# Kernel optimization log

Measured on AMD Instinct MI355X. Metric: run time of the kernel, lower is better.

The kernel has to match this reference:

```python
import jax, jax.numpy as jnp
import numpy as np
from jax import lax

N = 10000      # nodes (also LSTM seq_len, batch=1)
E = 640000     # edges
D = 256        # num_node_features
H = 512        # hidden_size (GIN out / LSTM input)
LH = 512       # lstm_hidden_size
BN_EPS = 1e-5


def setup_inputs() -> dict:
    key = jax.random.key(0)
    ks = jax.random.split(key, 20)
    def lin(k, out_d, in_d):
        s = 1.0 / np.sqrt(in_d)
        return jax.random.uniform(k, (out_d, in_d), jnp.float32, -s, s)
    def vec(k, d, fan):
        s = 1.0 / np.sqrt(fan)
        return jax.random.uniform(k, (d,), jnp.float32, -s, s)
    inp = {
        "x": jax.random.normal(ks[0], (N, D), jnp.float32),
        "edge_index": jax.random.randint(ks[1], (2, E), 0, N, jnp.int64),
        # GIN MLP: Linear(D,H) -> ReLU -> Linear(H,H)
        "w1": lin(ks[2], H, D), "b1": vec(ks[3], H, D),
        "w2": lin(ks[4], H, H), "b2": vec(ks[5], H, H),
        # BatchNorm1d(H) affine params (training-mode batch stats)
        "gamma": jnp.ones((H,), jnp.float32), "beta": jnp.zeros((H,), jnp.float32),
        # LSTM layer 0 (input H) and layer 1 (input LH); torch gate order i,f,g,o
        "w_ih0": lin(ks[6], 4 * LH, H), "w_hh0": lin(ks[7], 4 * LH, LH),
        "b_ih0": vec(ks[8], 4 * LH, LH), "b_hh0": vec(ks[9], 4 * LH, LH),
        "w_ih1": lin(ks[10], 4 * LH, LH), "w_hh1": lin(ks[11], 4 * LH, LH),
        "b_ih1": vec(ks[12], 4 * LH, LH), "b_hh1": vec(ks[13], 4 * LH, LH),
        # fc head
        "fc_w": lin(ks[14], 1, LH), "fc_b": vec(ks[15], 1, LH),
    }
    return inp


def _lstm_layer(xs, w_ih, w_hh, b_ih, b_hh):
    # xs: [T, in]; batch=1 squeezed. Precompute input projection as one big GEMM.
    Hh = w_hh.shape[1]
    pre = xs @ w_ih.T + b_ih + b_hh  # [T, 4H]
    def step(carry, p):
        h, c = carry
        gates = p + h @ w_hh.T
        i, f, g, o = jnp.split(gates, 4)
        i = jax.nn.sigmoid(i); f = jax.nn.sigmoid(f)
        g = jnp.tanh(g); o = jax.nn.sigmoid(o)
        c = f * c + i * g
        h = o * jnp.tanh(c)
        return (h, c), h
    init = (jnp.zeros((Hh,), xs.dtype), jnp.zeros((Hh,), xs.dtype))
    (h, c), hs = lax.scan(step, init, pre)
    return hs, h, c


def reference(x, edge_index, w1, b1, w2, b2, gamma, beta,
              w_ih0, w_hh0, b_ih0, b_hh0, w_ih1, w_hh1, b_ih1, b_hh1,
              fc_w, fc_b):
    n = x.shape[0]
    src, dst = edge_index[0], edge_index[1]
    # GINConv, eps=0: h_i = MLP(x_i + sum_{j->i} x_j)
    agg = jax.ops.segment_sum(x[src], dst, num_segments=n)
    h = x + agg
    h = jax.nn.relu(h @ w1.T + b1) @ w2.T + b2  # [N, H]
    # BatchNorm1d, training mode: biased batch stats over nodes
    mean = h.mean(axis=0)
    var = h.var(axis=0)
    h = (h - mean) * lax.rsqrt(var + BN_EPS) * gamma + beta
    h = jax.nn.relu(h)
    # dropout(p=0.5) treated as identity (eval mode, deterministic reference)
    # LSTM over the node sequence (batch=1), 2 stacked layers
    hs0, h0, c0 = _lstm_layer(h, w_ih0, w_hh0, b_ih0, b_hh0)
    hs1, h1, c1 = _lstm_layer(hs0, w_ih1, w_hh1, b_ih1, b_hh1)
    out = hs1 @ fc_w.T + fc_b          # [N, 1]
    out = out[:, 0][None, :]           # [1, N] after squeeze(2)
    h_n = jnp.stack([h0, h1])[:, None, :]  # [num_layers, 1, LH]
    c_n = jnp.stack([c0, c1])[:, None, :]
    return out, h_n, c_n
```

## Files before the change

### kernel.cpp

```cpp
#include <hip/hip_runtime.h>
#include <stdint.h>

#define N_NODES 10000
#define E_EDGES 640000
#define D_IN    256
#define H_DIM   512
#define K0      64
#define K1      128
#define RING    64

typedef unsigned short ushort_t;
typedef unsigned int   uint32;
typedef unsigned long long u64;

__device__ __forceinline__ float bf2f(ushort_t u) {
  union { uint32 i; float f; } v; v.i = ((uint32)u) << 16; return v.f;
}
__device__ __forceinline__ ushort_t f2bf(float f) {
  union { float f; uint32 i; } v; v.f = f;
  uint32 x = v.i;
  uint32 r = (x + 0x7FFFu + ((x >> 16) & 1u)) >> 16;
  return (ushort_t)r;
}

__device__ __forceinline__ float sigmoid_f(float x) {
  return 1.f / (1.f + __expf(-x));
}
__device__ __forceinline__ float tanh_f(float x) {
  x = fminf(10.f, fmaxf(-10.f, x));
  float e2 = __expf(2.f * x);
  return (e2 - 1.f) / (e2 + 1.f);
}

__device__ __forceinline__ u64 ld_c8(const u64* p) {
  return __hip_atomic_load(p, __ATOMIC_RELAXED, __HIP_MEMORY_SCOPE_AGENT);
}
__device__ __forceinline__ void st_c8(u64* p, float h, int flag) {
  u64 u = ((u64)(uint32)flag << 32) | (u64)__float_as_uint(h);
  __hip_atomic_store(p, u, __ATOMIC_RELAXED, __HIP_MEMORY_SCOPE_AGENT);
}
__device__ __forceinline__ void spin_relaxed(int* p, int target) {
  int guard = 0;
  while (__hip_atomic_load(p, __ATOMIC_RELAXED, __HIP_MEMORY_SCOPE_AGENT) < target) {
    __builtin_amdgcn_s_sleep(1);
    if (++guard > 100000000) break;
  }
  __atomic_signal_fence(__ATOMIC_ACQUIRE);
}

__global__ void k_zero(int* p) {
  p[blockIdx.x * 256 + threadIdx.x] = 0;
}

__global__ void k_detect(const int* eb, int* ctrl) {
  int v = eb[2 * (int)threadIdx.x + 1];
  if (v != 0) atomicOr(ctrl, 1);
}

__device__ __forceinline__ int edge_src(const int* eb, int flag, int e) {
  return flag ? eb[e] : eb[2 * e];
}
__device__ __forceinline__ int edge_dst(const int* eb, int flag, int e) {
  return flag ? eb[E_EDGES + e] : eb[2 * (E_EDGES + e)];
}

__global__ __launch_bounds__(256) void k_count(const int* eb, const int* ctrl, int* deg) {
  int e = blockIdx.x * 256 + threadIdx.x;
  if (e >= E_EDGES) return;
  int flag = ctrl[0];
  atomicAdd(&deg[edge_dst(eb, flag, e)], 1);
}

__global__ __launch_bounds__(1024) void k_prefix(const int* deg, int* off, int* cursor) {
  __shared__ int sums[1024];
  int tid = threadIdx.x;
  const int PER = 10;
  int base = tid * PER;
  int loc[PER];
  int s = 0;
  for (int i = 0; i < PER; i++) {
    int idx = base + i;
    int v = (idx < N_NODES) ? deg[idx] : 0;
    loc[i] = s; s += v;
  }
  sums[tid] = s;
  __syncthreads();
  for (int d = 1; d < 1024; d <<= 1) {
    int v = (tid >= d) ? sums[tid - d] : 0;
    __syncthreads();
    sums[tid] += v;
    __syncthreads();
  }
  int excl = (tid == 0) ? 0 : sums[tid - 1];
  for (int i = 0; i < PER; i++) {
    int idx = base + i;
    if (idx < N_NODES) { int o = excl + loc[i]; off[idx] = o; cursor[idx] = o; }
  }
  if (tid == 1023) off[N_NODES] = sums[1023];
}

// ... 59 lines not shown
    }
    __syncthreads();
  }
  float* Cf = (float*)Cout;
  ushort_t* Cb = (ushort_t*)Cout;
  #pragma unroll
  for (int i = 0; i < 4; i++) {
    int row = by * 64 + 16 * i + ty;
    if (row >= M) continue;
    #pragma unroll
    for (int j = 0; j < 4; j++) {
      int col = bn * 64 + 16 * j + tx;
      float b = bias1[col];
      if (TWOBIAS) b += bias2[col];
      float v = acc[i][j] + b;
      if (RELU) v = fmaxf(v, 0.f);
      if (OUTBF16) Cb[(size_t)row * Ncols + col] = f2bf(v);
      else         Cf[(size_t)row * Ncols + col] = v;
    }
  }
}

__global__ __launch_bounds__(256) void k_bnstats(const float* y2, float* colsum, float* colsumsq) {
  int b = blockIdx.x, tid = threadIdx.x;
  int r0 = b * 64, r1 = min(r0 + 64, N_NODES);
  float s0 = 0, q0 = 0, s1 = 0, q1 = 0;
  for (int r = r0; r < r1; r++) {
    float v0 = y2[(size_t)r * H_DIM + tid];
    float v1 = y2[(size_t)r * H_DIM + tid + 256];
    s0 += v0; q0 += v0 * v0; s1 += v1; q1 += v1 * v1;
  }
  atomicAdd(&colsum[tid], s0);        atomicAdd(&colsumsq[tid], q0);
  atomicAdd(&colsum[tid + 256], s1);  atomicAdd(&colsumsq[tid + 256], q1);
}

__global__ __launch_bounds__(256) void k_bnfin(float* colsum, float* colsumsq,
                                               const float* gamma, const float* beta) {
  int c = blockIdx.x * 256 + threadIdx.x;
  if (c >= H_DIM) return;
  float mean = colsum[c] * (1.f / N_NODES);
  float var  = colsumsq[c] * (1.f / N_NODES) - mean * mean;
  float sc = gamma[c] * rsqrtf(var + 1e-5f);
  float sh = beta[c] - mean * sc;
  colsum[c] = sc; colsumsq[c] = sh;
}

__global__ __launch_bounds__(256) void k_bnapply(float* y2, const float* sc, const float* sh) {
  size_t i = (size_t)blockIdx.x * 256 + threadIdx.x;
  int c = (int)(i & (H_DIM - 1));
  float v = y2[i] * sc[c] + sh[c];
  y2[i] = v > 0.f ? v : 0.f;
}

__global__ __launch_bounds__(256, 1) void k_lstm(const ushort_t* pre0, const float* w_hh0,
                                              const float* w_ih1, const float* w_hh1,
                                              const float* b_ih1, const float* b_hh1,
                                              u64* hs0c, u64* hs1c, float* hs1p,
                                              int* flags1, float* dout) {
  __shared__ float lds_in[2][512];
  __shared__ float lds_dots[32];
  __shared__ float lds_pre[2][32];
  int tid = threadIdx.x;
  int wave = tid >> 6, lane = tid & 63;
  int kp = lane & 7;
  int r = wave * 8 + (lane >> 3);
  int wg = blockIdx.x;

  float w_reg[64];
  float c_reg = 0.f;

  if (wg < K0) {
    int u0 = wg * 8;
    {
      int grow = (r >> 3) * H_DIM + u0 + (r & 7);
      const float* src = w_hh0 + (size_t)grow * H_DIM + kp * 64;
      #pragma unroll
      for (int i = 0; i < 16; i++) {
        int j0 = ((i + 2 * kp) & 15) * 4;
        float4 v = *(const float4*)(src + j0);
        w_reg[4 * i + 0] = v.x; w_reg[4 * i + 1] = v.y;
        w_reg[4 * i + 2] = v.z; w_reg[4 * i + 3] = v.w;
      }
    }
    float pf = 0.f;
    if (tid < 32)
      pf = bf2f(pre0[(tid >> 3) * H_DIM + u0 + (tid & 7)]);

    for (int t = 0; t < N_NODES; t++) {
      int phase = t & 1;
      if (t > 0) {
        const u64* pa = hs0c + ((t - 1) & (RING - 1)) * 512 + tid;
        const u64* pb = pa + 256;
        u64 ua, ub; int guard = 0;
        for (;;) {
          ua = ld_c8(pa); ub = ld_c8(pb);
          if (((int)(ua >> 32) == t && (int)(ub >> 32) == t) || ++guard > 100000000) break;
        }
        lds_in[0][tid]       = __uint_as_float((uint32)ua);
        lds_in[0][tid + 256] = __uint_as_float((uint32)ub);
      }
      if (tid < 32) lds_pre[phase][tid] = pf;
      __syncthreads();
      if (tid < 32 && t + 1 < N_NODES)
        pf = bf2f(pre0[(size_t)(t + 1) * 2048 + (tid >> 3) * H_DIM + u0 + (tid & 7)]);
      if ((t & 31) == 0 && t >= RING && tid < K1)
        spin_relaxed(&flags1[tid * 16], t - 32);
      if (t > 0) {
        const float* hrow = &lds_in[0][kp * 64];
        float dot = 0.f;
        #pragma unroll
        for (int i = 0; i < 16; i++) {
          int j0 = ((i + 2 * kp) & 15) * 4;
          float4 h4 = *(const float4*)(hrow + j0);
          dot += w_reg[4 * i] * h4.x + w_reg[4 * i + 1] * h4.y
               + w_reg[4 * i + 2] * h4.z + w_reg[4 * i + 3] * h4.w;
        }
        dot += __shfl_xor(dot, 1, 64);
        dot += __shfl_xor(dot, 2, 64);
        dot += __shfl_xor(dot, 4, 64);
        if (kp == 0) lds_dots[r] = dot;
      } else if (tid < 32) {
        lds_dots[tid] = 0.f;
      }
      __syncthreads();
      if (wave == 0) {
        float val = 0.f;
        if (lane < 32) {
          float pre = lds_dots[lane] + lds_pre[phase][lane];
          val = ((lane >> 3) == 2) ? tanh_f(pre) : sigmoid_f(pre);
        }
        int j = lane & 7;
        float ii = __shfl(val, j, 64);
        float ff = __shfl(val, 8 + j, 64);
        float gg = __shfl(val, 16 + j, 64);
        float oo = __shfl(val, 24 + j, 64);
        if (lane < 8) {
          c_reg = ff * c_reg + ii * gg;
          float hv = oo * tanh_f(c_reg);
          st_c8(hs0c + (t & (RING - 1)) * 512 + u0 + lane, hv, t + 1);
          if (t == N_NODES - 1) {
            dout[10000 + u0 + lane] = hv;
            dout[11024 + u0 + lane] = c_reg;
          }
        }
      }
    }
  } else {
    int wg1 = wg - K0;
    int u0 = wg1 * 4;
    int m = r >> 4;
    {
      int gj = r & 15;
      int grow = (gj >> 2) * H_DIM + u0 + (gj & 3);
      const float* src = (m ? w_hh1 : w_ih1) + (size_t)grow * H_DIM + kp * 64;
      #pragma unroll
      for (int i = 0; i < 16; i++) {
        int j0 = ((i + 2 * kp) & 15) * 4;
        float4 v = *(const float4*)(src + j0);
        w_reg[4 * i + 0] = v.x; w_reg[4 * i + 1] = v.y;
        w_reg[4 * i + 2] = v.z; w_reg[4 * i + 3] = v.w;
      }
    }
    if (tid < 16) {
      int g = tid >> 2, j = tid & 3;
      int grow = g * H_DIM + u0 + j;
      lds_pre[0][tid] = b_ih1[grow] + b_hh1[grow];
    }
    __syncthreads();

    for (int s = 0; s < N_NODES; s++) {
      {
        bool need1 = (s > 0);
        const u64* p0a = hs0c + (s & (RING - 1)) * 512 + tid;
        const u64* p0b = p0a + 256;
        const u64* p1a = hs1c + ((s - 1) & (RING - 1)) * 512 + tid;
        const u64* p1b = p1a + 256;
        u64 u0a, u0b, u1a, u1b; int guard = 0;
        for (;;) {
          u0a = ld_c8(p0a); u0b = ld_c8(p0b);
          u1a = ld_c8(p1a); u1b = ld_c8(p1b);
          bool ok0 = ((int)(u0a >> 32) == s + 1) && ((int)(u0b >> 32) == s + 1);
          bool ok1 = !need1 || (((int)(u1a >> 32) == s) && ((int)(u1b >> 32) == s));
          if ((ok0 && ok1) || ++guard > 100000000) break;
        }
        if (!need1) { u1a = 0; u1b = 0; }
        lds_in[0][tid]       = __uint_as_float((uint32)u0a);
        lds_in[0][tid + 256] = __uint_as_float((uint32)u0b);
        lds_in[1][tid]       = __uint_as_float((uint32)u1a);
        lds_in[1][tid + 256] = __uint_as_float((uint32)u1b);
      }
      __syncthreads();
      if (tid == 0)
        __hip_atomic_store(&flags1[wg1 * 16], s + 1, __ATOMIC_RELAXED, __HIP_MEMORY_SCOPE_AGENT);
      {
        const float* hrow = &lds_in[m][kp * 64];
        float dot = 0.f;
        #pragma unroll
        for (int i = 0; i < 16; i++) {
          int j0 = ((i + 2 * kp) & 15) * 4;
          float4 h4 = *(const float4*)(hrow + j0);
          dot += w_reg[4 * i] * h4.x + w_reg[4 * i + 1] * h4.y
               + w_reg[4 * i + 2] * h4.z + w_reg[4 * i + 3] * h4.w;
        }
        dot += __shfl_xor(dot, 1, 64);
        dot += __shfl_xor(dot, 2, 64);
        dot += __shfl_xor(dot, 4, 64);
        if (kp == 0) lds_dots[r] = dot;
      }
      __syncthreads();
      if (wave == 0) {
        float val = 0.f;
        if (lane < 16) {
          float pre = lds_dots[lane] + lds_dots[16 + lane] + lds_pre[0][lane];
          val = ((lane >> 2) == 2) ? tanh_f(pre) : sigmoid_f(pre);
        }
        int j = lane & 3;
        float ii = __shfl(val, j, 64);
        float ff = __shfl(val, 4 + j, 64);
        float gg = __shfl(val, 8 + j, 64);
        float oo = __shfl(val, 12 + j, 64);
        if (lane < 4) {
          c_reg = ff * c_reg + ii * gg;
          float hv = oo * tanh_f(c_reg);
          st_c8(hs1c + (s & (RING - 1)) * 512 + u0 + lane, hv, s + 1);
          hs1p[(size_t)s * H_DIM + u0 + lane] = hv;
          if (s == N_NODES - 1) {
            dout[10512 + u0 + lane] = hv;
            dout[11536 + u0 + lane] = c_reg;
          }
        }
      }
    }
  }
}

__global__ __launch_bounds__(256) void k_fc(const float* hs1, const float* fc_w,
                                            const float* fc_b, float* dout) {
  int row = blockIdx.x * 4 + (threadIdx.x >> 6);
  int lane = threadIdx.x & 63;
  float acc = 0.f;
  #pragma unroll
  for (int j = 0; j < 8; j++) {
    int c = lane + 64 * j;
    acc += hs1[(size_t)row * H_DIM + c] * fc_w[c];
  }
  for (int d = 32; d; d >>= 1) acc += __shfl_xor(acc, d, 64);
  if (lane == 0) dout[row] = acc + fc_b[0];
}

extern "C" void kernel_launch(void* const* d_in, const int* in_sizes, int n_in,
                              void* d_out, int out_size, void* d_ws, size_t ws_size,
                              hipStream_t stream) {
  const float* x     = (const float*)d_in[0];
  const int*   eb    = (const int*)d_in[1];
  const float* w1    = (const float*)d_in[2];
  const float* b1    = (const float*)d_in[3];
  const float* w2    = (const float*)d_in[4];
  const float* b2    = (const float*)d_in[5];
  const float* gamma = (const float*)d_in[6];
  const float* beta  = (const float*)d_in[7];
  const float* w_ih0 = (const float*)d_in[8];
  const float* w_hh0 = (const float*)d_in[9];
  const float* b_ih0 = (const float*)d_in[10];
  const float* b_hh0 = (const float*)d_in[11];
  const float* w_ih1 = (const float*)d_in[12];
  const float* w_hh1 = (const float*)d_in[13];
  const float* b_ih1 = (const float*)d_in[14];
  const float* b_hh1 = (const float*)d_in[15];
  const float* fc_w  = (const float*)d_in[16];
  const float* fc_b  = (const float*)d_in[17];
  float* dout = (float*)d_out;
  char* ws = (char*)d_ws;

  int*    ctrl     = (int*)(ws + 0);
  int*    flags1   = (int*)(ws + 256);
  float*  colsum   = (float*)(ws + 8448);
  float*  colsumsq = (float*)(ws + 10496);
  int*    deg      = (int*)(ws + 12544);
  u64*    hs0c     = (u64*)(ws + 57344);
  u64*    hs1c     = (u64*)(ws + 319488);
  float*  y1       = (float*)(ws + 581632);
  float*  y2       = (float*)(ws + 21061632);
  float*  h0       = y2;
  ushort_t* pre0   = (ushort_t*)(ws + 41541632);
  int*    off      = (int*)(ws + 41541632);
  int*    cursor   = (int*)(ws + 41582080);
  int*    csr      = (int*)(ws + 41622528);
  float*  hs1p     = y1;

  k_zero<<<56, 256, 0, stream>>>((int*)ws);
  k_detect<<<1, 64, 0, stream>>>(eb, ctrl);
  k_count<<<2500, 256, 0, stream>>>(eb, ctrl, deg);
  k_prefix<<<1, 1024, 0, stream>>>(deg, off, cursor);
  k_fill<<<2500, 256, 0, stream>>>(eb, ctrl, cursor, csr);
  k_agg<<<10000, 256, 0, stream>>>(x, off, csr, h0);

  dim3 g1(157, 8);
  k_gemm<256, true,  false, false><<<g1, 256, 0, stream>>>(h0, w1, b1, nullptr, y1, N_NODES, 512);
  dim3 g2(157, 8);
  k_gemm<512, false, false, false><<<g2, 256, 0, stream>>>(y1, w2, b2, nullptr, y2, N_NODES, 512);

  k_bnstats<<<157, 256, 0, stream>>>(y2, colsum, colsumsq);
  k_bnfin<<<2, 256, 0, stream>>>(colsum, colsumsq, gamma, beta);
  k_bnapply<<<20000, 256, 0, stream>>>(y2, colsum, colsumsq);

  dim3 g3(157, 32);
  k_gemm<512, false, true, true><<<g3, 256, 0, stream>>>(y2, w_ih0, b_ih0, b_hh0, pre0, N_NODES, 2048);

  k_lstm<<<192, 256, 0, stream>>>(pre0, w_hh0, w_ih1, w_hh1, b_ih1, b_hh1,
                                  hs0c, hs1c, hs1p, flags1, dout);
  k_fc<<<2500, 256, 0, stream>>>(hs1p, fc_w, fc_b, dout);
}
```

Baseline: 26.20 ms.

## Restructure persistent LSTM into single-wave workgroups with no LDS or barriers

Splits the persistent two-layer LSTM into 512 single-wavefront workgroups: 256 for layer 0 and 256 for layer 1, each owning 2 hidden units. Each lane holds an 8-wide slice of the weight rows in registers and reads its h slice straight from the flagged global ring, so the LDS staging and both __syncthreads per step go away. Dot products are reduced with full-wave shuffles, and the layer-0 throttle on layer-1 progress now uses a wave-wide vote every 16 steps. In exchange every wave polls the ring separately, which adds polling traffic, and the butterfly reductions cost more shuffles per step. The workspace offsets are also reshuffled.

Result: slower. 38.68 ms (+47.6%).

```diff
diff --git a/kernel.cpp b/kernel.cpp
--- a/kernel.cpp
+++ b/kernel.cpp
@@ -5,8 +5,6 @@
 #define E_EDGES 640000
 #define D_IN    256
 #define H_DIM   512
-#define K0      64
-#define K1      128
 #define RING    64
 
 typedef unsigned short ushort_t;
@@ -38,14 +36,6 @@
 __device__ __forceinline__ void st_c8(u64* p, float h, int flag) {
   u64 u = ((u64)(uint32)flag << 32) | (u64)__float_as_uint(h);
   __hip_atomic_store(p, u, __ATOMIC_RELAXED, __HIP_MEMORY_SCOPE_AGENT);
-}
-__device__ __forceinline__ void spin_relaxed(int* p, int target) {
-  int guard = 0;
-  while (__hip_atomic_load(p, __ATOMIC_RELAXED, __HIP_MEMORY_SCOPE_AGENT) < target) {
-    __builtin_amdgcn_s_sleep(1);
-    if (++guard > 100000000) break;
-  }
-  __atomic_signal_fence(__ATOMIC_ACQUIRE);
 }
 
 __global__ void k_zero(int* p) {
@@ -211,184 +201,220 @@
   y2[i] = v > 0.f ? v : 0.f;
 }
 
-__global__ __launch_bounds__(256, 1) void k_lstm(const ushort_t* pre0, const float* w_hh0,
+__global__ __launch_bounds__(64, 1) void k_lstm(const ushort_t* pre0, const float* w_hh0,
                                               const float* w_ih1, const float* w_hh1,
                                               const float* b_ih1, const float* b_hh1,
                                               u64* hs0c, u64* hs1c, float* hs1p,
                                               int* flags1, float* dout) {
-  __shared__ float lds_in[2][512];
-  __shared__ float lds_dots[32];
-  __shared__ float lds_pre[2][32];
-  int tid = threadIdx.x;
-  int wave = tid >> 6, lane = tid & 63;
-  int kp = lane & 7;
-  int r = wave * 8 + (lane >> 3);
+  int lane = threadIdx.x;
   int wg = blockIdx.x;
 
-  float w_reg[64];
-  float c_reg = 0.f;
-
-  if (wg < K0) {
-    int u0 = wg * 8;
-    {
-      int grow = (r >> 3) * H_DIM + u0 + (r & 7);
-      const float* src = w_hh0 + (size_t)grow * H_DIM + kp * 64;
+  if (wg < 256) {
+    int ubase = wg * 2;
+    float wr[8][8];
+    #pragma unroll
+    for (int rr = 0; rr < 8; rr++) {
+      int g = rr >> 1, u = rr & 1;
+      const float* src = w_hh0 + (size_t)(g * H_DIM + ubase + u) * H_DIM + lane * 8;
+      float4 a = *(const float4*)(src);
+      float4 b = *(const float4*)(src + 4);
+      wr[rr][0] = a.x; wr[rr][1] = a.y; wr[rr][2] = a.z; wr[rr][3] = a.w;
+      wr[rr][4] = b.x; wr[rr][5] = b.y; wr[rr][6] = b.z; wr[rr][7] = b.w;
+    }
+    uint32 ppk[4];
+    #pragma unroll
+    for (int g = 0; g < 4; g++)
+      ppk[g] = *(const uint32*)(pre0 + (size_t)0 * 2048 + g * H_DIM + ubase);
+    float c0 = 0.f, c1 = 0.f;
+
+    for (int t = 0; t < N_NODES; t++) {
+      float h[8];
+      if (t > 0) {
+        const u64* base = hs0c + (size_t)((t - 1) & (RING - 1)) * 512 + lane * 8;
+        u64 cc[8]; int guard = 0;
+        for (;;) {
+          #pragma unroll
+          for (int j = 0; j < 8; j++) cc[j] = ld_c8(base + j);
+          bool ok = true;
+          #pragma unroll
+          for (int j = 0; j < 8; j++) ok = ok && ((int)(cc[j] >> 32) == t);
+          if (ok || ++guard > 50000000) break;
+        }
+        #pragma unroll
+        for (int j = 0; j < 8; j++) h[j] = __uint_as_float((uint32)cc[j]);
+      } else {
+        #pragma unroll
+        for (int j = 0; j < 8; j++) h[j] = 0.f;
+      }
+      uint32 ppn[4];
+      if (t + 1 < N_NODES) {
+        #pragma unroll
+        for (int g = 0; g < 4; g++)
+          ppn[g] = *(const uint32*)(pre0 + (size_t)(t + 1) * 2048 + g * H_DIM + ubase);
+      } else {
+        #pragma unroll
+        for (int g = 0; g < 4; g++) ppn[g] = 0;
+      }
+      float d[8];
+      if (t > 0) {
+        #pragma unroll
+        for (int rr = 0; rr < 8; rr++) {
+          float s = 0.f;
+          #pragma unroll
+          for (int j = 0; j < 8; j++) s += wr[rr][j] * h[j];
+          d[rr] = s;
+        }
+        #pragma unroll
+        for (int rr = 0; rr < 8; rr++) {
+          #pragma unroll
+          for (int off = 1; off < 64; off <<= 1) d[rr] += __shfl_xor(d[rr], off, 64);
+        }
+      } else {
+        #pragma unroll
+        for (int rr = 0; rr < 8; rr++) d[rr] = 0.f;
+      }
+      float h0v, h1v;
+      {
+        float gi = d[0] + bf2f((ushort_t)(ppk[0] & 0xFFFF));
+        float gf = d[2] + bf2f((ushort_t)(ppk[1] & 0xFFFF));
+        float gg = d[4] + bf2f((ushort_t)(ppk[2] & 0xFFFF));
+        float go = d[6] + bf2f((ushort_t)(ppk[3] & 0xFFFF));
+        float ii = sigmoid_f(gi), ff = sigmoid_f(gf), g2 = tanh_f(gg), oo = sigmoid_f(go);
+        c0 = ff * c0 + ii * g2;
+        h0v = oo * tanh_f(c0);
+      }
+      {
+        float gi = d[1] + bf2f((ushort_t)(ppk[0] >> 16));
+        float gf = d[3] + bf2f((ushort_t)(ppk[1] >> 16));
+        float gg = d[5] + bf2f((ushort_t)(ppk[2] >> 16));
+        float go = d[7] + bf2f((ushort_t)(ppk[3] >> 16));
+        float ii = sigmoid_f(gi), ff = sigmoid_f(gf), g2 = tanh_f(gg), oo = sigmoid_f(go);
+        c1 = ff * c1 + ii * g2;
+        h1v = oo * tanh_f(c1);
+      }
+      if (lane < 2) {
+        float hv = lane ? h1v : h0v;
+        st_c8(hs0c + (size_t)(t & (RING - 1)) * 512 + ubase + lane, hv, t + 1);
+        if (t == N_NODES - 1) {
+          dout[10000 + ubase + lane] = hv;
+          dout[11024 + ubase + lane] = lane ? c1 : c0;
+        }
+      }
+      if ((t & 15) == 0 && t >= 48) {
+        int tgt = t - 32;
+        int g2_ = 0;
+        for (;;) {
+          int m0 = __hip_atomic_load(&flags1[lane * 4 + 0], __ATOMIC_RELAXED, __HIP_MEMORY_SCOPE_AGENT);
+          int m1 = __hip_atomic_load(&flags1[lane * 4 + 1], __ATOMIC_RELAXED, __HIP_MEMORY_SCOPE_AGENT);
+          int m2 = __hip_atomic_load(&flags1[lane * 4 + 2], __ATOMIC_RELAXED, __HIP_MEMORY_SCOPE_AGENT);
+          int m3 = __hip_atomic_load(&flags1[lane * 4 + 3], __ATOMIC_RELAXED, __HIP_MEMORY_SCOPE_AGENT);
+          bool myok = (m0 >= tgt) && (m1 >= tgt) && (m2 >= tgt) && (m3 >= tgt);
+          if (__all(myok) || ++g2_ > 5000000) break;
+          __builtin_amdgcn_s_sleep(1);
+        }
+      }
       #pragma unroll
-      for (int i = 0; i < 16; i++) {
-        int j0 = ((i + 2 * kp) & 15) * 4;
-        float4 v = *(const float4*)(src + j0);
-        w_reg[4 * i + 0] = v.x; w_reg[4 * i + 1] = v.y;
-        w_reg[4 * i + 2] = v.z; w_reg[4 * i + 3] = v.w;
-      }
-    }
-    float pf = 0.f;
-    if (tid < 32)
-      pf = bf2f(pre0[(tid >> 3) * H_DIM + u0 + (tid & 7)]);
-
-    for (int t = 0; t < N_NODES; t++) {
-      int phase = t & 1;
-      if (t > 0) {
-        const u64* pa = hs0c + ((t - 1) & (RING - 1)) * 512 + tid;
-        const u64* pb = pa + 256;
-        u64 ua, ub; int guard = 0;
-        for (;;) {
-          ua = ld_c8(pa); ub = ld_c8(pb);
-          if (((int)(ua >> 32) == t && (int)(ub >> 32) == t) || ++guard > 100000000) break;
-        }
-        lds_in[0][tid]       = __uint_as_float((uint32)ua);
-        lds_in[0][tid + 256] = __uint_as_float((uint32)ub);
-      }
-      if (tid < 32) lds_pre[phase][tid] = pf;
-      __syncthreads();
-      if (tid < 32 && t + 1 < N_NODES)
-        pf = bf2f(pre0[(size_t)(t + 1) * 2048 + (tid >> 3) * H_DIM + u0 + (tid & 7)]);
-      if ((t & 31) == 0 && t >= RING && tid < K1)
-        spin_relaxed(&flags1[tid * 16], t - 32);
-      if (t > 0) {
-        const float* hrow = &lds_in[0][kp * 64];
-        float dot = 0.f;
-        #pragma unroll
-        for (int i = 0; i < 16; i++) {
-          int j0 = ((i + 2 * kp) & 15) * 4;
-          float4 h4 = *(const float4*)(hrow + j0);
-          dot += w_reg[4 * i] * h4.x + w_reg[4 * i + 1] * h4.y
-               + w_reg[4 * i + 2] * h4.z + w_reg[4 * i + 3] * h4.w;
-        }
-        dot += __shfl_xor(dot, 1, 64);
-        dot += __shfl_xor(dot, 2, 64);
-        dot += __shfl_xor(dot, 4, 64);
-        if (kp == 0) lds_dots[r] = dot;
-      } else if (tid < 32) {
-        lds_dots[tid] = 0.f;
-      }
-      __syncthreads();
-      if (wave == 0) {
-        float val = 0.f;
-        if (lane < 32) {
-          float pre = lds_dots[lane] + lds_pre[phase][lane];
-          val = ((lane >> 3) == 2) ? tanh_f(pre) : sigmoid_f(pre);
-        }
-        int j = lane & 7;
-        float ii = __shfl(val, j, 64);
-        float ff = __shfl(val, 8 + j, 64);
-        float gg = __shfl(val, 16 + j, 64);
-        float oo = __shfl(val, 24 + j, 64);
-        if (lane < 8) {
-          c_reg = ff * c_reg + ii * gg;
-          float hv = oo * tanh_f(c_reg);
-          st_c8(hs0c + (t & (RING - 1)) * 512 + u0 + lane, hv, t + 1);
-          if (t == N_NODES - 1) {
-            dout[10000 + u0 + lane] = hv;
-            dout[11024 + u0 + lane] = c_reg;
+      for (int g = 0; g < 4; g++) ppk[g] = ppn[g];
+    }
+  } else {
+    int wg1 = wg - 256;
+    int ubase = wg1 * 2;
+    float wi[8][8], wh[8][8], bb[8];
+    #pragma unroll
+    for (int rr = 0; rr < 8; rr++) {
+      int g = rr >> 1, u = rr & 1;
+      size_t grow = (size_t)(g * H_DIM + ubase + u);
+      const float* si = w_ih1 + grow * H_DIM + lane * 8;
+      const float* sh = w_hh1 + grow * H_DIM + lane * 8;
+      float4 a = *(const float4*)(si);
+      float4 b = *(const float4*)(si + 4);
+      wi[rr][0] = a.x; wi[rr][1] = a.y; wi[rr][2] = a.z; wi[rr][3] = a.w;
+      wi[rr][4] = b.x; wi[rr][5] = b.y; wi[rr][6] = b.z; wi[rr][7] = b.w;
+      float4 c = *(const float4*)(sh);
+      float4 e = *(const float4*)(sh + 4);
+      wh[rr][0] = c.x; wh[rr][1] = c.y; wh[rr][2] = c.z; wh[rr][3] = c.w;
+      wh[rr][4] = e.x; wh[rr][5] = e.y; wh[rr][6] = e.z; wh[rr][7] = e.w;
+      bb[rr] = b_ih1[grow] + b_hh1[grow];
+    }
+    float c0 = 0.f, c1 = 0.f;
+
+    for (int s = 0; s < N_NODES; s++) {
+      float h0[8], h1[8];
+      {
+        const u64* b0 = hs0c + (size_t)(s & (RING - 1)) * 512 + lane * 8;
+        const u64* b1 = hs1c + (size_t)((s - 1) & (RING - 1)) * 512 + lane * 8;
+        u64 a0[8], a1[8]; int guard = 0;
+        if (s > 0) {
+          for (;;) {
+            #pragma unroll
+            for (int j = 0; j < 8; j++) a0[j] = ld_c8(b0 + j);
+            #pragma unroll
+            for (int j = 0; j < 8; j++) a1[j] = ld_c8(b1 + j);
+            bool ok = true;
+            #pragma unroll
+            for (int j = 0; j < 8; j++) ok = ok && ((int)(a0[j] >> 32) == s + 1);
+            #pragma unroll
+            for (int j = 0; j < 8; j++) ok = ok && ((int)(a1[j] >> 32) == s);
+            if (ok || ++guard > 50000000) break;
           }
-        }
-      }
-    }
-  } else {
-    int wg1 = wg - K0;
-    int u0 = wg1 * 4;
-    int m = r >> 4;
-    {
-      int gj = r & 15;
-      int grow = (gj >> 2) * H_DIM + u0 + (gj & 3);
-      const float* src = (m ? w_hh1 : w_ih1) + (size_t)grow * H_DIM + kp * 64;
+          #pragma unroll
+          for (int j = 0; j < 8; j++) { h0[j] = __uint_as_float((uint32)a0[j]); h1[j] = __uint_as_float((uint32)a1[j]); }
+        } else {
+          for (;;) {
+            #pragma unroll
+            for (int j = 0; j < 8; j++) a0[j] = ld_c8(b0 + j);
+            bool ok = true;
+            #pragma unroll
+            for (int j = 0; j < 8; j++) ok = ok && ((int)(a0[j] >> 32) == 1);
+            if (ok || ++guard > 50000000) break;
+          }
+          #pragma unroll
+          for (int j = 0; j < 8; j++) { h0[j] = __uint_as_float((uint32)a0[j]); h1[j] = 0.f; }
+        }
+      }
+      float d[8];
       #pragma unroll
-      for (int i = 0; i < 16; i++) {
-        int j0 = ((i + 2 * kp) & 15) * 4;
-        float4 v = *(const float4*)(src + j0);
-        w_reg[4 * i + 0] = v.x; w_reg[4 * i + 1] = v.y;
-        w_reg[4 * i + 2] = v.z; w_reg[4 * i + 3] = v.w;
-      }
-    }
-    if (tid < 16) {
-      int g = tid >> 2, j = tid & 3;
-      int grow = g * H_DIM + u0 + j;
-      lds_pre[0][tid] = b_ih1[grow] + b_hh1[grow];
-    }
-    __syncthreads();
-
-    for (int s = 0; s < N_NODES; s++) {
+      for (int rr = 0; rr < 8; rr++) {
+        float acc = 0.f;
+        #pragma unroll
+        for (int j = 0; j < 8; j++) acc += wi[rr][j] * h0[j];
+        #pragma unroll
+        for (int j = 0; j < 8; j++) acc += wh[rr][j] * h1[j];
+        d[rr] = acc;
+      }
+      #pragma unroll
+      for (int rr = 0; rr < 8; rr++) {
+        #pragma unroll
+        for (int off = 1; off < 64; off <<= 1) d[rr] += __shfl_xor(d[rr], off, 64);
+      }
+      float h0v, h1v;
       {
-        bool need1 = (s > 0);
-        const u64* p0a = hs0c + (s & (RING - 1)) * 512 + tid;
-        const u64* p0b = p0a + 256;
-        const u64* p1a = hs1c + ((s - 1) & (RING - 1)) * 512 + tid;
-        const u64* p1b = p1a + 256;
-        u64 u0a, u0b, u1a, u1b; int guard = 0;
-        for (;;) {
-          u0a = ld_c8(p0a); u0b = ld_c8(p0b);
-          u1a = ld_c8(p1a); u1b = ld_c8(p1b);
-          bool ok0 = ((int)(u0a >> 32) == s + 1) && ((int)(u0b >> 32) == s + 1);
-          bool ok1 = !need1 || (((int)(u1a >> 32) == s) && ((int)(u1b >> 32) == s));
-          if ((ok0 && ok1) || ++guard > 100000000) break;
-        }
-        if (!need1) { u1a = 0; u1b = 0; }
-        lds_in[0][tid]       = __uint_as_float((uint32)u0a);
-        lds_in[0][tid + 256] = __uint_as_float((uint32)u0b);
-        lds_in[1][tid]       = __uint_as_float((uint32)u1a);
-        lds_in[1][tid + 256] = __uint_as_float((uint32)u1b);
-      }
-      __syncthreads();
-      if (tid == 0)
-        __hip_atomic_store(&flags1[wg1 * 16], s + 1, __ATOMIC_RELAXED, __HIP_MEMORY_SCOPE_AGENT);
+        float ii = sigmoid_f(d[0] + bb[0]);
+        float ff = sigmoid_f(d[2] + bb[2]);
+        float g2 = tanh_f(d[4] + bb[4]);
+        float oo = sigmoid_f(d[6] + bb[6]);
+        c0 = ff * c0 + ii * g2;
+        h0v = oo * tanh_f(c0);
+      }
       {
-        const float* hrow = &lds_in[m][kp * 64];
-        float dot = 0.f;
-        #pragma unroll
-        for (int i = 0; i < 16; i++) {
-          int j0 = ((i + 2 * kp) & 15) * 4;
-          float4 h4 = *(const float4*)(hrow + j0);
-          dot += w_reg[4 * i] * h4.x + w_reg[4 * i + 1] * h4.y
-               + w_reg[4 * i + 2] * h4.z + w_reg[4 * i + 3] * h4.w;
-        }
-        dot += __shfl_xor(dot, 1, 64);
-        dot += __shfl_xor(dot, 2, 64);
-        dot += __shfl_xor(dot, 4, 64);
-        if (kp == 0) lds_dots[r] = dot;
-      }
-      __syncthreads();
-      if (wave == 0) {
-        float val = 0.f;
-        if (lane < 16) {
-          float pre = lds_dots[lane] + lds_dots[16 + lane] + lds_pre[0][lane];
-          val = ((lane >> 2) == 2) ? tanh_f(pre) : sigmoid_f(pre);
-        }
-        int j = lane & 3;
-        float ii = __shfl(val, j, 64);
-        float ff = __shfl(val, 4 + j, 64);
-        float gg = __shfl(val, 8 + j, 64);
-        float oo = __shfl(val, 12 + j, 64);
-        if (lane < 4) {
-          c_reg = ff * c_reg + ii * gg;
-          float hv = oo * tanh_f(c_reg);
-          st_c8(hs1c + (s & (RING - 1)) * 512 + u0 + lane, hv, s + 1);
-          hs1p[(size_t)s * H_DIM + u0 + lane] = hv;
-          if (s == N_NODES - 1) {
-            dout[10512 + u0 + lane] = hv;
-            dout[11536 + u0 + lane] = c_reg;
-          }
-        }
-      }
+        float ii = sigmoid_f(d[1] + bb[1]);
+        float ff = sigmoid_f(d[3] + bb[3]);
+        float g2 = tanh_f(d[5] + bb[5]);
+        float oo = sigmoid_f(d[7] + bb[7]);
+        c1 = ff * c1 + ii * g2;
+        h1v = oo * tanh_f(c1);
+      }
+      if (lane < 2) {
+        float hv = lane ? h1v : h0v;
+        st_c8(hs1c + (size_t)(s & (RING - 1)) * 512 + ubase + lane, hv, s + 1);
+        hs1p[(size_t)s * H_DIM + ubase + lane] = hv;
+        if (s == N_NODES - 1) {
+          dout[10512 + ubase + lane] = hv;
+          dout[11536 + ubase + lane] = lane ? c1 : c0;
+        }
+      }
+      if (lane == 0)
+        __hip_atomic_store(&flags1[wg1], s + 1, __ATOMIC_RELAXED, __HIP_MEMORY_SCOPE_AGENT);
     }
   }
 }
@@ -432,19 +458,19 @@
   char* ws = (char*)d_ws;
 
   int*    ctrl     = (int*)(ws + 0);
-  int*    flags1   = (int*)(ws + 256);
-  float*  colsum   = (float*)(ws + 8448);
-  float*  colsumsq = (float*)(ws + 10496);
-  int*    deg      = (int*)(ws + 12544);
-  u64*    hs0c     = (u64*)(ws + 57344);
-  u64*    hs1c     = (u64*)(ws + 319488);
-  float*  y1       = (float*)(ws + 581632);
-  float*  y2       = (float*)(ws + 21061632);
+  int*    flags1   = (int*)(ws + 1024);
+  float*  colsum   = (float*)(ws + 4096);
+  float*  colsumsq = (float*)(ws + 6144);
+  int*    deg      = (int*)(ws + 8192);
+  u64*    hs0c     = (u64*)(ws + 65536);
+  u64*    hs1c     = (u64*)(ws + 327680);
+  float*  y1       = (float*)(ws + 589824);
+  float*  y2       = (float*)(ws + 21069824);
   float*  h0       = y2;
-  ushort_t* pre0   = (ushort_t*)(ws + 41541632);
-  int*    off      = (int*)(ws + 41541632);
-  int*    cursor   = (int*)(ws + 41582080);
-  int*    csr      = (int*)(ws + 41622528);
+  ushort_t* pre0   = (ushort_t*)(ws + 41549824);
+  int*    off      = (int*)(ws + 41549824);
+  int*    cursor   = (int*)(ws + 41589828);
+  int*    csr      = (int*)(ws + 41629828);
   float*  hs1p     = y1;
 
   k_zero<<<56, 256, 0, stream>>>((int*)ws);
@@ -466,7 +492,7 @@
   dim3 g3(157, 32);
   k_gemm<512, false, true, true><<<g3, 256, 0, stream>>>(y2, w_ih0, b_ih0, b_hh0, pre0, N_NODES, 2048);
 
-  k_lstm<<<192, 256, 0, stream>>>(pre0, w_hh0, w_ih1, w_hh1, b_ih1, b_hh1,
-                                  hs0c, hs1c, hs1p, flags1, dout);
+  k_lstm<<<512, 64, 0, stream>>>(pre0, w_hh0, w_ih1, w_hh1, b_ih1, b_hh1,
+                                 hs0c, hs1c, hs1p, flags1, dout);
   k_fc<<<2500, 256, 0, stream>>>(hs1p, fc_w, fc_b, dout);
 }
```

## Remove second block barrier per LSTM step by computing gates inside each wave

Applied to the files above, without the earlier changes.

Reworks the persistent LSTM kernel so each wave owns whole hidden units (two units per wave in layer 0, one in layer 1). All four gate dot products for a unit are reduced inside the wave with shuffles, and the cell update runs there too. This removes the per-step LDS gate exchange and the second __syncthreads, and the h buffer is double-buffered in LDS. Layer-1 flags are packed densely instead of padded to 16 ints, and the layer-0 backpressure check changes to poll them with a different target and sleep. The gate activations are now computed redundantly on many lanes, and the denser flag layout may cause more contention on the polled lines.

After: 33.58 ms. 1.28x slower.

```diff
diff --git a/kernel.cpp b/kernel.cpp
--- a/kernel.cpp
+++ b/kernel.cpp
@@ -38,14 +38,6 @@
 __device__ __forceinline__ void st_c8(u64* p, float h, int flag) {
   u64 u = ((u64)(uint32)flag << 32) | (u64)__float_as_uint(h);
   __hip_atomic_store(p, u, __ATOMIC_RELAXED, __HIP_MEMORY_SCOPE_AGENT);
-}
-__device__ __forceinline__ void spin_relaxed(int* p, int target) {
-  int guard = 0;
-  while (__hip_atomic_load(p, __ATOMIC_RELAXED, __HIP_MEMORY_SCOPE_AGENT) < target) {
-    __builtin_amdgcn_s_sleep(1);
-    if (++guard > 100000000) break;
-  }
-  __atomic_signal_fence(__ATOMIC_ACQUIRE);
 }
 
 __global__ void k_zero(int* p) {
@@ -216,177 +208,168 @@
                                               const float* b_ih1, const float* b_hh1,
                                               u64* hs0c, u64* hs1c, float* hs1p,
                                               int* flags1, float* dout) {
-  __shared__ float lds_in[2][512];
-  __shared__ float lds_dots[32];
-  __shared__ float lds_pre[2][32];
+  __shared__ float lds_h[2][1024];
   int tid = threadIdx.x;
   int wave = tid >> 6, lane = tid & 63;
-  int kp = lane & 7;
-  int r = wave * 8 + (lane >> 3);
   int wg = blockIdx.x;
 
-  float w_reg[64];
-  float c_reg = 0.f;
-
   if (wg < K0) {
-    int u0 = wg * 8;
+    int u_w = wg * 8 + wave * 2;
+    int rr = lane >> 3, kp = lane & 7;
+    int g_r = rr >> 1, u_r = rr & 1;
+    float w_reg[64];
     {
-      int grow = (r >> 3) * H_DIM + u0 + (r & 7);
-      const float* src = w_hh0 + (size_t)grow * H_DIM + kp * 64;
+      const float* src = w_hh0 + (size_t)(g_r * H_DIM + u_w + u_r) * H_DIM + kp * 64;
       #pragma unroll
       for (int i = 0; i < 16; i++) {
         int j0 = ((i + 2 * kp) & 15) * 4;
         float4 v = *(const float4*)(src + j0);
-        w_reg[4 * i + 0] = v.x; w_reg[4 * i + 1] = v.y;
-        w_reg[4 * i + 2] = v.z; w_reg[4 * i + 3] = v.w;
-      }
-    }
-    float pf = 0.f;
-    if (tid < 32)
-      pf = bf2f(pre0[(tid >> 3) * H_DIM + u0 + (tid & 7)]);
+        w_reg[4*i+0]=v.x; w_reg[4*i+1]=v.y; w_reg[4*i+2]=v.z; w_reg[4*i+3]=v.w;
+      }
+    }
+    int myu = u_w + (lane & 1);
+    float ppk[4];
+    #pragma unroll
+    for (int g = 0; g < 4; g++)
+      ppk[g] = bf2f(pre0[(size_t)0 * 2048 + g * H_DIM + myu]);
+    float c_reg = 0.f;
 
     for (int t = 0; t < N_NODES; t++) {
-      int phase = t & 1;
+      float* Lh = lds_h[t & 1];
       if (t > 0) {
-        const u64* pa = hs0c + ((t - 1) & (RING - 1)) * 512 + tid;
+        const u64* pa = hs0c + (size_t)((t-1) & (RING-1)) * 512 + tid;
         const u64* pb = pa + 256;
         u64 ua, ub; int guard = 0;
         for (;;) {
           ua = ld_c8(pa); ub = ld_c8(pb);
-          if (((int)(ua >> 32) == t && (int)(ub >> 32) == t) || ++guard > 100000000) break;
-        }
-        lds_in[0][tid]       = __uint_as_float((uint32)ua);
-        lds_in[0][tid + 256] = __uint_as_float((uint32)ub);
-      }
-      if (tid < 32) lds_pre[phase][tid] = pf;
+          if (((int)(ua>>32) == t && (int)(ub>>32) == t) || ++guard > 100000000) break;
+        }
+        Lh[tid]       = __uint_as_float((uint32)ua);
+        Lh[tid + 256] = __uint_as_float((uint32)ub);
+      }
       __syncthreads();
-      if (tid < 32 && t + 1 < N_NODES)
-        pf = bf2f(pre0[(size_t)(t + 1) * 2048 + (tid >> 3) * H_DIM + u0 + (tid & 7)]);
-      if ((t & 31) == 0 && t >= RING && tid < K1)
-        spin_relaxed(&flags1[tid * 16], t - 32);
+      float ppn[4];
+      if (t + 1 < N_NODES) {
+        #pragma unroll
+        for (int g = 0; g < 4; g++)
+          ppn[g] = bf2f(pre0[(size_t)(t+1) * 2048 + g * H_DIM + myu]);
+      } else { ppn[0]=ppn[1]=ppn[2]=ppn[3]=0.f; }
+      if ((t & 31) == 0 && t >= 32 && tid < K1) {
+        int tgt = t - 31, guard = 0;
+        while (__hip_atomic_load(&flags1[tid], __ATOMIC_RELAXED, __HIP_MEMORY_SCOPE_AGENT) < tgt) {
+          __builtin_amdgcn_s_sleep(2);
+          if (++guard > 50000000) break;
+        }
+      }
+      float d = 0.f;
       if (t > 0) {
-        const float* hrow = &lds_in[0][kp * 64];
-        float dot = 0.f;
+        const float* hrow = Lh + kp * 64;
         #pragma unroll
         for (int i = 0; i < 16; i++) {
           int j0 = ((i + 2 * kp) & 15) * 4;
           float4 h4 = *(const float4*)(hrow + j0);
-          dot += w_reg[4 * i] * h4.x + w_reg[4 * i + 1] * h4.y
-               + w_reg[4 * i + 2] * h4.z + w_reg[4 * i + 3] * h4.w;
-        }
-        dot += __shfl_xor(dot, 1, 64);
-        dot += __shfl_xor(dot, 2, 64);
-        dot += __shfl_xor(dot, 4, 64);
-        if (kp == 0) lds_dots[r] = dot;
-      } else if (tid < 32) {
-        lds_dots[tid] = 0.f;
-      }
-      __syncthreads();
-      if (wave == 0) {
-        float val = 0.f;
-        if (lane < 32) {
-          float pre = lds_dots[lane] + lds_pre[phase][lane];
-          val = ((lane >> 3) == 2) ? tanh_f(pre) : sigmoid_f(pre);
-        }
-        int j = lane & 7;
-        float ii = __shfl(val, j, 64);
-        float ff = __shfl(val, 8 + j, 64);
-        float gg = __shfl(val, 16 + j, 64);
-        float oo = __shfl(val, 24 + j, 64);
-        if (lane < 8) {
-          c_reg = ff * c_reg + ii * gg;
-          float hv = oo * tanh_f(c_reg);
-          st_c8(hs0c + (t & (RING - 1)) * 512 + u0 + lane, hv, t + 1);
-          if (t == N_NODES - 1) {
-            dout[10000 + u0 + lane] = hv;
-            dout[11024 + u0 + lane] = c_reg;
-          }
-        }
-      }
+          d += w_reg[4*i]*h4.x + w_reg[4*i+1]*h4.y + w_reg[4*i+2]*h4.z + w_reg[4*i+3]*h4.w;
+        }
+        d += __shfl_xor(d, 1, 64);
+        d += __shfl_xor(d, 2, 64);
+        d += __shfl_xor(d, 4, 64);
+      }
+      int u = lane & 1;
+      float gi = __shfl(d, 8 * u, 64)      + ppk[0];
+      float gf = __shfl(d, 16 + 8 * u, 64) + ppk[1];
+      float gg = __shfl(d, 32 + 8 * u, 64) + ppk[2];
+      float go = __shfl(d, 48 + 8 * u, 64) + ppk[3];
+      float ii = sigmoid_f(gi), ff = sigmoid_f(gf), gz = tanh_f(gg), oo = sigmoid_f(go);
+      c_reg = ff * c_reg + ii * gz;
+      float hv = oo * tanh_f(c_reg);
+      if (lane < 2) {
+        st_c8(hs0c + (size_t)(t & (RING-1)) * 512 + myu, hv, t + 1);
+        if (t == N_NODES - 1) {
+          dout[10000 + myu] = hv;
+          dout[11024 + myu] = c_reg;
+        }
+      }
+      ppk[0]=ppn[0]; ppk[1]=ppn[1]; ppk[2]=ppn[2]; ppk[3]=ppn[3];
     }
   } else {
     int wg1 = wg - K0;
-    int u0 = wg1 * 4;
-    int m = r >> 4;
+    int unit = wg1 * 4 + wave;
+    int g_r = lane >> 4, seg = lane & 15;
+    float w_reg[64];
     {
-      int gj = r & 15;
-      int grow = (gj >> 2) * H_DIM + u0 + (gj & 3);
-      const float* src = (m ? w_hh1 : w_ih1) + (size_t)grow * H_DIM + kp * 64;
+      size_t grow = (size_t)(g_r * H_DIM + unit);
+      const float* base = (seg < 8) ? (w_ih1 + grow * H_DIM) : (w_hh1 + grow * H_DIM - 512);
       #pragma unroll
       for (int i = 0; i < 16; i++) {
-        int j0 = ((i + 2 * kp) & 15) * 4;
-        float4 v = *(const float4*)(src + j0);
-        w_reg[4 * i + 0] = v.x; w_reg[4 * i + 1] = v.y;
-        w_reg[4 * i + 2] = v.z; w_reg[4 * i + 3] = v.w;
-      }
-    }
-    if (tid < 16) {
-      int g = tid >> 2, j = tid & 3;
-      int grow = g * H_DIM + u0 + j;
-      lds_pre[0][tid] = b_ih1[grow] + b_hh1[grow];
-    }
-    __syncthreads();
+        int j0 = ((i + seg) & 15) * 4;
+        float4 v = *(const float4*)(base + seg * 64 + j0);
+        w_reg[4*i+0]=v.x; w_reg[4*i+1]=v.y; w_reg[4*i+2]=v.z; w_reg[4*i+3]=v.w;
+      }
+    }
+    float bb[4];
+    #pragma unroll
+    for (int g = 0; g < 4; g++) bb[g] = b_ih1[g * H_DIM + unit] + b_hh1[g * H_DIM + unit];
+    float c_reg = 0.f;
 
     for (int s = 0; s < N_NODES; s++) {
+      float* Lh = lds_h[s & 1];
       {
-        bool need1 = (s > 0);
-        const u64* p0a = hs0c + (s & (RING - 1)) * 512 + tid;
+        const u64* p0a = hs0c + (size_t)(s & (RING-1)) * 512 + tid;
         const u64* p0b = p0a + 256;
-        const u64* p1a = hs1c + ((s - 1) & (RING - 1)) * 512 + tid;
-        const u64* p1b = p1a + 256;
-        u64 u0a, u0b, u1a, u1b; int guard = 0;
-        for (;;) {
-          u0a = ld_c8(p0a); u0b = ld_c8(p0b);
-          u1a = ld_c8(p1a); u1b = ld_c8(p1b);
-          bool ok0 = ((int)(u0a >> 32) == s + 1) && ((int)(u0b >> 32) == s + 1);
-          bool ok1 = !need1 || (((int)(u1a >> 32) == s) && ((int)(u1b >> 32) == s));
-          if ((ok0 && ok1) || ++guard > 100000000) break;
-        }
-        if (!need1) { u1a = 0; u1b = 0; }
-        lds_in[0][tid]       = __uint_as_float((uint32)u0a);
-        lds_in[0][tid + 256] = __uint_as_float((uint32)u0b);
-        lds_in[1][tid]       = __uint_as_float((uint32)u1a);
-        lds_in[1][tid + 256] = __uint_as_float((uint32)u1b);
+        u64 ua, ub; int guard = 0;
+        if (s > 0) {
+          const u64* p1a = hs1c + (size_t)((s-1) & (RING-1)) * 512 + tid;
+          const u64* p1b = p1a + 256;
+          u64 va, vb;
+          for (;;) {
+            ua = ld_c8(p0a); ub = ld_c8(p0b); va = ld_c8(p1a); vb = ld_c8(p1b);
+            bool ok = ((int)(ua>>32) == s+1) && ((int)(ub>>32) == s+1)
+                   && ((int)(va>>32) == s)   && ((int)(vb>>32) == s);
+            if (ok || ++guard > 100000000) break;
+          }
+          Lh[512 + tid]       = __uint_as_float((uint32)va);
+          Lh[512 + tid + 256] = __uint_as_float((uint32)vb);
+        } else {
+          for (;;) {
+            ua = ld_c8(p0a); ub = ld_c8(p0b);
+            if (((int)(ua>>32) == 1 && (int)(ub>>32) == 1) || ++guard > 100000000) break;
+          }
+          Lh[512 + tid]       = 0.f;
+          Lh[512 + tid + 256] = 0.f;
+        }
+        Lh[tid]       = __uint_as_float((uint32)ua);
+        Lh[tid + 256] = __uint_as_float((uint32)ub);
       }
       __syncthreads();
       if (tid == 0)
-        __hip_atomic_store(&flags1[wg1 * 16], s + 1, __ATOMIC_RELAXED, __HIP_MEMORY_SCOPE_AGENT);
+        __hip_atomic_store(&flags1[wg1], s + 1, __ATOMIC_RELAXED, __HIP_MEMORY_SCOPE_AGENT);
+      float d = 0.f;
       {
-        const float* hrow = &lds_in[m][kp * 64];
-        float dot = 0.f;
+        const float* hrow = Lh + seg * 64;
         #pragma unroll
         for (int i = 0; i < 16; i++) {
-          int j0 = ((i + 2 * kp) & 15) * 4;
+          int j0 = ((i + seg) & 15) * 4;
           float4 h4 = *(const float4*)(hrow + j0);
-          dot += w_reg[4 * i] * h4.x + w_reg[4 * i + 1] * h4.y
-               + w_reg[4 * i + 2] * h4.z + w_reg[4 * i + 3] * h4.w;
-        }
-        dot += __shfl_xor(dot, 1, 64);
-        dot += __shfl_xor(dot, 2, 64);
-        dot += __shfl_xor(dot, 4, 64);
-        if (kp == 0) lds_dots[r] = dot;
-      }
-      __syncthreads();
-      if (wave == 0) {
-        float val = 0.f;
-        if (lane < 16) {
-          float pre = lds_dots[lane] + lds_dots[16 + lane] + lds_pre[0][lane];
-          val = ((lane >> 2) == 2) ? tanh_f(pre) : sigmoid_f(pre);
-        }
-        int j = lane & 3;
-        float ii = __shfl(val, j, 64);
-        float ff = __shfl(val, 4 + j, 64);
-        float gg = __shfl(val, 8 + j, 64);
-        float oo = __shfl(val, 12 + j, 64);
-        if (lane < 4) {
-          c_reg = ff * c_reg + ii * gg;
-          float hv = oo * tanh_f(c_reg);
-          st_c8(hs1c + (s & (RING - 1)) * 512 + u0 + lane, hv, s + 1);
-          hs1p[(size_t)s * H_DIM + u0 + lane] = hv;
-          if (s == N_NODES - 1) {
-            dout[10512 + u0 + lane] = hv;
-            dout[11536 + u0 + lane] = c_reg;
-          }
+          d += w_reg[4*i]*h4.x + w_reg[4*i+1]*h4.y + w_reg[4*i+2]*h4.z + w_reg[4*i+3]*h4.w;
+        }
+      }
+      d += __shfl_xor(d, 1, 64);
+      d += __shfl_xor(d, 2, 64);
+      d += __shfl_xor(d, 4, 64);
+      d += __shfl_xor(d, 8, 64);
+      float gi = __shfl(d, 0, 64)  + bb[0];
+      float gf = __shfl(d, 16, 64) + bb[1];
+      float gg = __shfl(d, 32, 64) + bb[2];
+      float go = __shfl(d, 48, 64) + bb[3];
+      float ii = sigmoid_f(gi), ff = sigmoid_f(gf), gz = tanh_f(gg), oo = sigmoid_f(go);
+      c_reg = ff * c_reg + ii * gz;
+      float hv = oo * tanh_f(c_reg);
+      if (lane == 0) {
+        st_c8(hs1c + (size_t)(s & (RING-1)) * 512 + unit, hv, s + 1);
+        hs1p[(size_t)s * H_DIM + unit] = hv;
+        if (s == N_NODES - 1) {
+          dout[10512 + unit] = hv;
+          dout[11536 + unit] = c_reg;
         }
       }
     }
@@ -432,19 +415,19 @@
   char* ws = (char*)d_ws;
 
   int*    ctrl     = (int*)(ws + 0);
-  int*    flags1   = (int*)(ws + 256);
-  float*  colsum   = (float*)(ws + 8448);
-  float*  colsumsq = (float*)(ws + 10496);
-  int*    deg      = (int*)(ws + 12544);
-  u64*    hs0c     = (u64*)(ws + 57344);
-  u64*    hs1c     = (u64*)(ws + 319488);
-  float*  y1       = (float*)(ws + 581632);
-  float*  y2       = (float*)(ws + 21061632);
+  int*    flags1   = (int*)(ws + 1024);
+  float*  colsum   = (float*)(ws + 4096);
+  float*  colsumsq = (float*)(ws + 6144);
+  int*    deg      = (int*)(ws + 8192);
+  u64*    hs0c     = (u64*)(ws + 65536);
+  u64*    hs1c     = (u64*)(ws + 327680);
+  float*  y1       = (float*)(ws + 589824);
+  float*  y2       = (float*)(ws + 21069824);
   float*  h0       = y2;
-  ushort_t* pre0   = (ushort_t*)(ws + 41541632);
-  int*    off      = (int*)(ws + 41541632);
-  int*    cursor   = (int*)(ws + 41582080);
-  int*    csr      = (int*)(ws + 41622528);
+  ushort_t* pre0   = (ushort_t*)(ws + 41549824);
+  int*    off      = (int*)(ws + 41549824);
+  int*    cursor   = (int*)(ws + 41589828);
+  int*    csr      = (int*)(ws + 41629828);
   float*  hs1p     = y1;
 
   k_zero<<<56, 256, 0, stream>>>((int*)ws);
```

## Replace per-element ring polling with arrival-counter epoch mailboxes in persistent LSTM

Applied to the files above, without the earlier changes.

The persistent two-layer LSTM kernel previously had every thread poll tagged hidden-state slots in a global ring, and layer-0 blocks gated on 128 per-block progress flags. Now each block bumps an atomic arrival counter per timestep. The last arriver resets a future counter slot and writes an epoch value into a per-block mailbox, so blocks first spin on a single mailbox word before reading the ring. The aim is to cut cross-CU polling traffic and contention on the serial recurrence critical path, at the cost of an extra atomic round-trip plus a broadcast write on every step.

Result: slower. 34.99 ms (+33.6%).

```diff
diff --git a/kernel.cpp b/kernel.cpp
--- a/kernel.cpp
+++ b/kernel.cpp
@@ -39,13 +39,11 @@
   u64 u = ((u64)(uint32)flag << 32) | (u64)__float_as_uint(h);
   __hip_atomic_store(p, u, __ATOMIC_RELAXED, __HIP_MEMORY_SCOPE_AGENT);
 }
-__device__ __forceinline__ void spin_relaxed(int* p, int target) {
-  int guard = 0;
-  while (__hip_atomic_load(p, __ATOMIC_RELAXED, __HIP_MEMORY_SCOPE_AGENT) < target) {
-    __builtin_amdgcn_s_sleep(1);
-    if (++guard > 100000000) break;
-  }
-  __atomic_signal_fence(__ATOMIC_ACQUIRE);
+__device__ __forceinline__ int ld_flag(const int* p) {
+  return __hip_atomic_load(p, __ATOMIC_RELAXED, __HIP_MEMORY_SCOPE_AGENT);
+}
+__device__ __forceinline__ void st_flag(int* p, int v) {
+  __hip_atomic_store(p, v, __ATOMIC_RELAXED, __HIP_MEMORY_SCOPE_AGENT);
 }
 
 __global__ void k_zero(int* p) {
@@ -215,7 +213,8 @@
                                               const float* w_ih1, const float* w_hh1,
                                               const float* b_ih1, const float* b_hh1,
                                               u64* hs0c, u64* hs1c, float* hs1p,
-                                              int* flags1, float* dout) {
+                                              int* ep0_mail, int* ep1_mail,
+                                              int* arrive0, int* arrive1, float* dout) {
   __shared__ float lds_in[2][512];
   __shared__ float lds_dots[32];
   __shared__ float lds_pre[2][32];
@@ -248,9 +247,14 @@
     for (int t = 0; t < N_NODES; t++) {
       int phase = t & 1;
       if (t > 0) {
-        const u64* pa = hs0c + ((t - 1) & (RING - 1)) * 512 + tid;
+        int guard = 0;
+        while (ld_flag(&ep0_mail[wg]) < t) {
+          __builtin_amdgcn_s_sleep(1);
+          if (++guard > 100000000) break;
+        }
+        const u64* pa = hs0c + (size_t)((t - 1) & (RING - 1)) * 512 + tid;
         const u64* pb = pa + 256;
-        u64 ua, ub; int guard = 0;
+        u64 ua, ub; guard = 0;
         for (;;) {
           ua = ld_c8(pa); ub = ld_c8(pb);
           if (((int)(ua >> 32) == t && (int)(ub >> 32) == t) || ++guard > 100000000) break;
@@ -262,8 +266,13 @@
       __syncthreads();
       if (tid < 32 && t + 1 < N_NODES)
         pf = bf2f(pre0[(size_t)(t + 1) * 2048 + (tid >> 3) * H_DIM + u0 + (tid & 7)]);
-      if ((t & 31) == 0 && t >= RING && tid < K1)
-        spin_relaxed(&flags1[tid * 16], t - 32);
+      if ((t & 15) == 0 && t >= 32) {
+        int tgt = t - 16, guard = 0;
+        while (ld_flag(&ep1_mail[wg]) < tgt) {
+          __builtin_amdgcn_s_sleep(2);
+          if (++guard > 50000000) break;
+        }
+      }
       if (t > 0) {
         const float* hrow = &lds_in[0][kp * 64];
         float dot = 0.f;
@@ -296,11 +305,24 @@
         if (lane < 8) {
           c_reg = ff * c_reg + ii * gg;
           float hv = oo * tanh_f(c_reg);
-          st_c8(hs0c + (t & (RING - 1)) * 512 + u0 + lane, hv, t + 1);
+          st_c8(hs0c + (size_t)(t & (RING - 1)) * 512 + u0 + lane, hv, t + 1);
           if (t == N_NODES - 1) {
             dout[10000 + u0 + lane] = hv;
             dout[11024 + u0 + lane] = c_reg;
           }
+        }
+        int lastf = 0;
+        if (lane == 0) {
+          int old = __hip_atomic_fetch_add(&arrive0[t & (RING - 1)], 1,
+                                           __ATOMIC_RELAXED, __HIP_MEMORY_SCOPE_AGENT);
+          lastf = (old == K0 - 1) ? 1 : 0;
+        }
+        lastf = __shfl(lastf, 0, 64);
+        if (lastf) {
+          if (lane == 0) st_flag(&arrive0[(t + 32) & (RING - 1)], 0);
+          #pragma unroll
+          for (int m = 0; m < 3; m++)
+            st_flag(&ep0_mail[lane + 64 * m], t + 1);
         }
       }
     }
@@ -329,12 +351,19 @@
 
     for (int s = 0; s < N_NODES; s++) {
       {
+        int guard = 0;
+        for (;;) {
+          int e0 = ld_flag(&ep0_mail[wg]);
+          int e1 = (s > 0) ? ld_flag(&ep1_mail[wg]) : s;
+          if ((e0 >= s + 1 && e1 >= s) || ++guard > 100000000) break;
+          __builtin_amdgcn_s_sleep(1);
+        }
         bool need1 = (s > 0);
-        const u64* p0a = hs0c + (s & (RING - 1)) * 512 + tid;
+        const u64* p0a = hs0c + (size_t)(s & (RING - 1)) * 512 + tid;
         const u64* p0b = p0a + 256;
-        const u64* p1a = hs1c + ((s - 1) & (RING - 1)) * 512 + tid;
+        const u64* p1a = hs1c + (size_t)((s - 1) & (RING - 1)) * 512 + tid;
         const u64* p1b = p1a + 256;
-        u64 u0a, u0b, u1a, u1b; int guard = 0;
+        u64 u0a, u0b, u1a, u1b; guard = 0;
         for (;;) {
           u0a = ld_c8(p0a); u0b = ld_c8(p0b);
           u1a = ld_c8(p1a); u1b = ld_c8(p1b);
@@ -349,8 +378,6 @@
         lds_in[1][tid + 256] = __uint_as_float((uint32)u1b);
       }
       __syncthreads();
-      if (tid == 0)
-        __hip_atomic_store(&flags1[wg1 * 16], s + 1, __ATOMIC_RELAXED, __HIP_MEMORY_SCOPE_AGENT);
       {
         const float* hrow = &lds_in[m][kp * 64];
         float dot = 0.f;
@@ -381,12 +408,25 @@
         if (lane < 4) {
           c_reg = ff * c_reg + ii * gg;
           float hv = oo * tanh_f(c_reg);
-          st_c8(hs1c + (s & (RING - 1)) * 512 + u0 + lane, hv, s + 1);
+          st_c8(hs1c + (size_t)(s & (RING - 1)) * 512 + u0 + lane, hv, s + 1);
           hs1p[(size_t)s * H_DIM + u0 + lane] = hv;
           if (s == N_NODES - 1) {
             dout[10512 + u0 + lane] = hv;
             dout[11536 + u0 + lane] = c_reg;
           }
+        }
+        int lastf = 0;
+        if (lane == 0) {
+          int old = __hip_atomic_fetch_add(&arrive1[s & (RING - 1)], 1,
+                                           __ATOMIC_RELAXED, __HIP_MEMORY_SCOPE_AGENT);
+          lastf = (old == K1 - 1) ? 1 : 0;
+        }
+        lastf = __shfl(lastf, 0, 64);
+        if (lastf) {
+          if (lane == 0) st_flag(&arrive1[(s + 32) & (RING - 1)], 0);
+          #pragma unroll
+          for (int mm = 0; mm < 3; mm++)
+            st_flag(&ep1_mail[lane + 64 * mm], s + 1);
         }
       }
     }
@@ -432,19 +472,22 @@
   char* ws = (char*)d_ws;
 
   int*    ctrl     = (int*)(ws + 0);
-  int*    flags1   = (int*)(ws + 256);
-  float*  colsum   = (float*)(ws + 8448);
-  float*  colsumsq = (float*)(ws + 10496);
-  int*    deg      = (int*)(ws + 12544);
-  u64*    hs0c     = (u64*)(ws + 57344);
-  u64*    hs1c     = (u64*)(ws + 319488);
-  float*  y1       = (float*)(ws + 581632);
-  float*  y2       = (float*)(ws + 21061632);
+  int*    ep0_mail = (int*)(ws + 1024);
+  int*    ep1_mail = (int*)(ws + 2048);
+  int*    arrive0  = (int*)(ws + 3072);
+  int*    arrive1  = (int*)(ws + 3584);
+  float*  colsum   = (float*)(ws + 4096);
+  float*  colsumsq = (float*)(ws + 6144);
+  int*    deg      = (int*)(ws + 8192);
+  u64*    hs0c     = (u64*)(ws + 65536);
+  u64*    hs1c     = (u64*)(ws + 327680);
+  float*  y1       = (float*)(ws + 589824);
+  float*  y2       = (float*)(ws + 21069824);
   float*  h0       = y2;
-  ushort_t* pre0   = (ushort_t*)(ws + 41541632);
-  int*    off      = (int*)(ws + 41541632);
-  int*    cursor   = (int*)(ws + 41582080);
-  int*    csr      = (int*)(ws + 41622528);
+  ushort_t* pre0   = (ushort_t*)(ws + 41549824);
+  int*    off      = (int*)(ws + 41549824);
+  int*    cursor   = (int*)(ws + 41589828);
+  int*    csr      = (int*)(ws + 41629828);
   float*  hs1p     = y1;
 
   k_zero<<<56, 256, 0, stream>>>((int*)ws);
@@ -467,6 +510,7 @@
   k_gemm<512, false, true, true><<<g3, 256, 0, stream>>>(y2, w_ih0, b_ih0, b_hh0, pre0, N_NODES, 2048);
 
   k_lstm<<<192, 256, 0, stream>>>(pre0, w_hh0, w_ih1, w_hh1, b_ih1, b_hh1,
-                                  hs0c, hs1c, hs1p, flags1, dout);
+                                  hs0c, hs1c, hs1p, ep0_mail, ep1_mail,
+                                  arrive0, arrive1, dout);
   k_fc<<<2500, 256, 0, stream>>>(hs1p, fc_w, fc_b, dout);
 }
```
